# Optimization experiments

Measured on AMD Instinct MI355X. Metric: run time of the kernel, lower is better.

The kernel has to match this reference:

```python
import jax, jax.numpy as jnp
import numpy as np

B, S, HID = 1, 4096, 2304
NH, NKV, HD = 8, 4, 256
SW = 2048                 # sliding window (layer_idx=0 -> active)
SOFTCAP = 50.0
SCALE = 256.0 ** -0.5     # query_pre_attn_scalar ** -0.5
THETA = 10000.0
NEG = -1e30


def rotate_half(x):
    x1, x2 = jnp.split(x, 2, axis=-1)
    return jnp.concatenate([-x2, x1], axis=-1)


def setup_inputs() -> dict:
    key = jax.random.key(0)
    ks = jax.random.split(key, 5)
    hidden_states = jax.random.normal(ks[0], (B, S, HID), jnp.float32)
    position_ids = jnp.tile(jnp.arange(S, dtype=jnp.int32)[None, :], (B, 1))
    Wq = 0.02 * jax.random.normal(ks[1], (NH * HD, HID), jnp.float32)
    Wk = 0.02 * jax.random.normal(ks[2], (NKV * HD, HID), jnp.float32)
    Wv = 0.02 * jax.random.normal(ks[3], (NKV * HD, HID), jnp.float32)
    Wo = 0.02 * jax.random.normal(ks[4], (HID, NH * HD), jnp.float32)
    return {"hidden_states": hidden_states, "position_ids": position_ids,
            "Wq": Wq, "Wk": Wk, "Wv": Wv, "Wo": Wo}


def reference(hidden_states, position_ids, Wq, Wk, Wv, Wo):
    b, s, _ = hidden_states.shape
    # fused QKV projections (torch Linear: y = x @ W.T)
    q = jnp.einsum('bsh,oh->bso', hidden_states, Wq).reshape(b, s, NH, HD).transpose(0, 2, 1, 3)
    k = jnp.einsum('bsh,oh->bso', hidden_states, Wk).reshape(b, s, NKV, HD).transpose(0, 2, 1, 3)
    v = jnp.einsum('bsh,oh->bso', hidden_states, Wv).reshape(b, s, NKV, HD).transpose(0, 2, 1, 3)

    # rotary embedding
    inv_freq = 1.0 / (THETA ** (jnp.arange(0, HD, 2, dtype=jnp.float32) / HD))
    freqs = position_ids.astype(jnp.float32)[:, :, None] * inv_freq[None, None, :]  # [b,s,hd/2]
    emb = jnp.concatenate([freqs, freqs], axis=-1)                                  # [b,s,hd]
    cos = jnp.cos(emb)[:, None, :, :]  # [b,1,s,hd]
    sin = jnp.sin(emb)[:, None, :, :]
    q = q * cos + rotate_half(q) * sin
    k = k * cos + rotate_half(k) * sin

    # GQA: repeat kv heads
    groups = NH // NKV
    k = jnp.repeat(k, groups, axis=1)  # [b,nh,s,hd]
    v = jnp.repeat(v, groups, axis=1)

    scores = jnp.einsum('bhqd,bhkd->bhqk', q, k) * SCALE
    scores = SOFTCAP * jnp.tanh(scores / SOFTCAP)  # logit softcapping

    i = jnp.arange(s)[:, None]
    j = jnp.arange(s)[None, :]
    mask = (j <= i) & ((i - j) < SW)               # causal + sliding window
    scores = jnp.where(mask[None, None], scores, NEG)

    attn = jax.nn.softmax(scores, axis=-1)
    out = jnp.einsum('bhqk,bhkd->bhqd', attn, v)
    out = out.transpose(0, 2, 1, 3).reshape(b, s, NH * HD)
    return jnp.einsum('bso,ho->bsh', out, Wo)
```

## Files before the change

kernel.cpp:

```cpp
#include <hip/hip_runtime.h>
#include <hip/hip_bf16.h>

typedef __attribute__((ext_vector_type(8))) short short8;
typedef __attribute__((ext_vector_type(4))) short short4v;
typedef __attribute__((ext_vector_type(4))) float floatx4;
typedef __attribute__((ext_vector_type(8))) _Float16 half8;

#define S_LEN 4096
#define HIDDEN 2304
#define NHEADS 8
#define NKVH 4
#define HDIM 256
#define SWIN 2048

static __device__ __forceinline__ short bf16bits(float x) {
    __hip_bfloat16 h = __float2bfloat16(x);
    return __builtin_bit_cast(short, h);
}
static __device__ __forceinline__ float bits2f(short b) {
    return __bfloat162float(__builtin_bit_cast(__hip_bfloat16, b));
}

static __device__ __forceinline__ void gload_lds16(const short* g, short* l) {
    __builtin_amdgcn_global_load_lds((const __attribute__((address_space(1))) void*)g,
                                     (__attribute__((address_space(3))) void*)l,
                                     16, 0, 0);
}

__global__ __launch_bounds__(256) void cast_f32_bf16(const float* __restrict__ in,
                                                     short* __restrict__ out, int n4) {
    int i = blockIdx.x * 256 + threadIdx.x;
    if (i >= n4) return;
    float4 v = ((const float4*)in)[i];
    short4v o;
    o.x = bf16bits(v.x); o.y = bf16bits(v.y); o.z = bf16bits(v.z); o.w = bf16bits(v.w);
    ((short4v*)out)[i] = o;
}

__global__ __launch_bounds__(256) void cast_wqkv(const float* __restrict__ Wq,
                                                 const float* __restrict__ Wk,
                                                 const float* __restrict__ Wv,
                                                 short* __restrict__ dst) {
    const int NQ4 = 1179648, NK4 = 589824;
    int i = blockIdx.x * 256 + threadIdx.x;
    const float4* src;
    if (i < NQ4)            src = (const float4*)Wq + i;
    else if (i < NQ4 + NK4) src = (const float4*)Wk + (i - NQ4);
    else                    src = (const float4*)Wv + (i - NQ4 - NK4);
    float4 v = *src;
    short4v o;
    o.x = bf16bits(v.x); o.y = bf16bits(v.y); o.z = bf16bits(v.z); o.w = bf16bits(v.w);
    ((short4v*)dst)[i] = o;
}

template<int MODE>
__global__ __launch_bounds__(256) void gemm_lds(const short* __restrict__ A,
                                                const short* __restrict__ B,
                                                void* __restrict__ Cp,
                                                int M, int N, int K, int ldc)
{
    __shared__ __align__(16) short lA[128 * 32];
    __shared__ __align__(16) short lB[128 * 32];
    int tid  = threadIdx.x;
    int lane = tid & 63;
    int wave = tid >> 6;
    int col  = lane & 15;
    int quad = lane >> 4;
    int m_base = blockIdx.y * 128;
    int n_base = blockIdx.x * 128;
    int wm = (wave >> 1) * 64;
    int wn = (wave & 1) * 64;

    int srow = wave * 32 + (lane >> 2);
    int scol = (lane & 3) * 8;
    const short* gA0 = A + (size_t)(m_base + srow) * K + scol;
    const short* gA1 = gA0 + (size_t)16 * K;
    const short* gB0 = B + (size_t)(n_base + srow) * K + scol;
    const short* gB1 = gB0 + (size_t)16 * K;
    short* lA0 = lA + wave * 1024;
    short* lB0 = lB + wave * 1024;

    floatx4 acc[4][4] = {};

    for (int k0 = 0; k0 < K; k0 += 32) {
        __syncthreads();
        gload_lds16(gA0 + k0, lA0);
        gload_lds16(gA1 + k0, lA0 + 512);
        gload_lds16(gB0 + k0, lB0);
        gload_lds16(gB1 + k0, lB0 + 512);
        __syncthreads();

        short8 af[4], bf[4];
        #pragma unroll
        for (int t = 0; t < 4; ++t) {
            af[t] = *(const short8*)(lA + (wm + t*16 + col) * 32 + quad * 8);
            bf[t] = *(const short8*)(lB + (wn + t*16 + col) * 32 + quad * 8);
        }
        #pragma unroll
        for (int mt = 0; mt < 4; ++mt)
            #pragma unroll
            for (int nt = 0; nt < 4; ++nt)
                acc[mt][nt] = __builtin_amdgcn_mfma_f32_16x16x32_bf16(af[mt], bf[nt], acc[mt][nt], 0, 0, 0);
    }

    #pragma unroll
    for (int mt = 0; mt < 4; ++mt) {
        #pragma unroll
        for (int nt = 0; nt < 4; ++nt) {
            int n  = n_base + wn + nt*16 + col;
            int m0 = m_base + wm + mt*16 + quad*4;
            if (MODE == 0) {
                short* C = (short*)Cp;
                #pragma unroll
                for (int r = 0; r < 4; ++r)
                    C[(size_t)(m0 + r) * ldc + n] = bf16bits(acc[mt][nt][r]);
            } else {
                float* C = (float*)Cp;
                #pragma unroll
                for (int r = 0; r < 4; ++r)
                    C[(size_t)(m0 + r) * ldc + n] = acc[mt][nt][r];
            }
        }
    }
}

__global__ __launch_bounds__(256) void gemm_qkv(const short* __restrict__ A,
                                                const short* __restrict__ B,
                                                short* __restrict__ QKV,
                                                short* __restrict__ Vt)
{
    __shared__ __align__(16) short lA[128 * 32];
    __shared__ __align__(16) short lB[128 * 32];
    const int K = HIDDEN;
    int tid  = threadIdx.x;
    int lane = tid & 63;
    int wave = tid >> 6;
    int col  = lane & 15;
    int quad = lane >> 4;
    int m_base = blockIdx.y * 128;
    int n_base = blockIdx.x * 128;
    int wm = (wave >> 1) * 64;
    int wn = (wave & 1) * 64;

    int srow = wave * 32 + (lane >> 2);
    int scol = (lane & 3) * 8;
    const short* gA0 = A + (size_t)(m_base + srow) * K + scol;
    const short* gA1 = gA0 + (size_t)16 * K;
    const short* gB0 = B + (size_t)(n_base + srow) * K + scol;
    const short* gB1 = gB0 + (size_t)16 * K;
    short* lA0 = lA + wave * 1024;
    short* lB0 = lB + wave * 1024;

    floatx4 acc[4][4] = {};

    for (int k0 = 0; k0 < K; k0 += 32) {
        __syncthreads();
        gload_lds16(gA0 + k0, lA0);
        gload_lds16(gA1 + k0, lA0 + 512);
        gload_lds16(gB0 + k0, lB0);
        gload_lds16(gB1 + k0, lB0 + 512);
        __syncthreads();

        short8 af[4], bf[4];
        #pragma unroll
        for (int t = 0; t < 4; ++t) {
            af[t] = *(const short8*)(lA + (wm + t*16 + col) * 32 + quad * 8);
            bf[t] = *(const short8*)(lB + (wn + t*16 + col) * 32 + quad * 8);
        }
        #pragma unroll
        for (int mt = 0; mt < 4; ++mt)
            #pragma unroll
            for (int nt = 0; nt < 4; ++nt)
                acc[mt][nt] = __builtin_amdgcn_mfma_f32_16x16x32_bf16(af[mt], bf[nt], acc[mt][nt], 0, 0, 0);
    }

    #pragma unroll
    for (int mt = 0; mt < 4; ++mt) {
        #pragma unroll
        for (int nt = 0; nt < 4; ++nt) {
            int n  = n_base + wn + nt*16 + col;
            int m0 = m_base + wm + mt*16 + quad*4;
            if (n_base + wn + nt*16 < 3072) {
                #pragma unroll
                for (int r = 0; r < 4; ++r)
                    QKV[(size_t)(m0 + r) * 4096 + n] = bf16bits(acc[mt][nt][r]);
            } else {
                short4v v;
                v.x = bf16bits(acc[mt][nt][0]);
                v.y = bf16bits(acc[mt][nt][1]);
                v.z = bf16bits(acc[mt][nt][2]);
                v.w = bf16bits(acc[mt][nt][3]);
                *(short4v*)(Vt + (size_t)(n - 3072) * 4096 + m0) = v;
            }
        }
    }
}

__global__ __launch_bounds__(256) void rope_kernel(short* __restrict__ QKV,
                                                   const int* __restrict__ pos)
{
    int t = blockIdx.x * 256 + threadIdx.x;
    int d   = t & 127;
    int rem = t >> 7;
    int hh  = rem % 12;
    int s   = rem / 12;
    float p   = (float)pos[s];
    float inv = __expf(-9.210340371976184f * ((float)d * (1.0f/128.0f)));
    float ang = p * inv;
    float sn, cs;
    sincosf(ang, &sn, &cs);
    short* row = QKV + (size_t)s * 4096 + hh * 256;
    float x1 = bits2f(row[d]);
    float x2 = bits2f(row[d + 128]);
    row[d]       = bf16bits(x1 * cs - x2 * sn);
    row[d + 128] = bf16bits(x2 * cs + x1 * sn);
}

__global__ __launch_bounds__(512) void attn_kernel(const short* __restrict__ QKV,
                                                   const short* __restrict__ Vt,
                                                   _Float16* __restrict__ Opart,
                                                   float* __restrict__ Psp)
{
    __shared__ __align__(16) short lK[2][32 * 256];
    __shared__ __align__(16) short lV[2][256 * 32];
    __shared__ __align__(16) short lP[8][32 * 64];
    int tid  = threadIdx.x;
    int lane = tid & 63;
    int wave = tid >> 6;
    int col  = lane & 15;
    int quad = lane >> 4;
    int bid0 = blockIdx.x;
    int bid  = (bid0 & 7) * 32 + (bid0 >> 3);
    int g     = bid >> 6;
    int chunk = (bid >> 1) & 31;
    int half  = bid & 1;
    int h     = g * 2 + (wave >> 2);
    int qb = chunk * 128;
    int q0 = qb + (wave & 3) * 32;

    short* lPw = lP[wave];

    short8 qf[2][8];
    #pragma unroll
    for (int mt = 0; mt < 2; ++mt) {
        const short* Qrow = QKV + (size_t)(q0 + mt*16 + col) * 4096 + h * 256;
        #pragma unroll
        for (int c = 0; c < 8; ++c)
            qf[mt][c] = *(const short8*)(Qrow + c*32 + quad*8);
    }

    int l5 = lane >> 5;
    int segK = lane & 31;
    const short* pK[2];
    int dKoff[2];
    #pragma unroll
    for (int i = 0; i < 2; ++i) {
        int p = wave * 2 + i;
        int row = 2 * p + l5;
        pK[i] = QKV + (size_t)row * 4096 + 2048 + g * 256 + ((segK ^ (row & 7)) << 3);
        dKoff[i] = p * 512;
    }
    const short* pV[2];
    int dVoff[2];
    #pragma unroll
    for (int i = 0; i < 2; ++i) {
        int row = wave * 32 + i * 16 + (lane >> 2);
        pV[i] = Vt + (size_t)(g * 256 + row) * 4096 + (((lane & 3) ^ ((row >> 1) & 3)) << 3);
        dVoff[i] = wave * 1024 + i * 512;
    }

    floatx4 o[2][16] = {};
    float psum[2][4] = {};

    int kb_lo = qb - (SWIN - 1);
    if (kb_lo < 0) kb_lo = 0;
    kb_lo &= ~31;
    int T  = ((qb + 128) - kb_lo) >> 5;
    int T0 = T >> 1;
    int kb_beg = kb_lo + (half ? T0 * 32 : 0);
    int kb_end = kb_lo + (half ? T * 32 : T0 * 32);

    #pragma unroll
    for (int i = 0; i < 2; ++i)
        gload_lds16(pK[i] + (size_t)kb_beg * 4096, &lK[0][dKoff[i]]);
    #pragma unroll
    for (int i = 0; i < 2; ++i)
        gload_lds16(pV[i] + kb_beg, &lV[0][dVoff[i]]);
    __syncthreads();

    int cur = 0;
    for (int kb = kb_beg; kb < kb_end; kb += 32) {
        int nkb = kb + 32;
        if (nkb < kb_end) {
            #pragma unroll
            for (int i = 0; i < 2; ++i)
                gload_lds16(pK[i] + (size_t)nkb * 4096, &lK[cur ^ 1][dKoff[i]]);
            #pragma unroll
            for (int i = 0; i < 2; ++i)
                gload_lds16(pV[i] + nkb, &lV[cur ^ 1][dVoff[i]]);
        }

        bool deadv = (kb > q0 + 31) || (kb + 2078 < q0);
        if (!deadv) {
            bool full = (kb + 32 <= q0) && (kb >= q0 - 2016);
            const short* Kb = lK[cur];
            const short* Vb = lV[cur];

            floatx4 sc[2][2] = {};
            __builtin_amdgcn_s_setprio(1);
            #pragma unroll
            for (int c = 0; c < 8; ++c) {
                int off = (c*32 + quad*8) ^ ((col & 7) << 3);
                short8 kf0 = *(const short8*)(Kb + col * 256 + off);
                short8 kf1 = *(const short8*)(Kb + (16 + col) * 256 + off);
                #pragma unroll
                for (int mt = 0; mt < 2; ++mt) {
                    sc[mt][0] = __builtin_amdgcn_mfma_f32_16x16x32_bf16(qf[mt][c], kf0, sc[mt][0], 0, 0, 0);
                    sc[mt][1] = __builtin_amdgcn_mfma_f32_16x16x32_bf16(qf[mt][c], kf1, sc[mt][1], 0, 0, 0);
                }
            }
            __builtin_amdgcn_s_setprio(0);

#define CONV_BODY(MASKED)                                                           \
            _Pragma("unroll")                                                       \
            for (int mt = 0; mt < 2; ++mt)                                          \
                _Pragma("unroll")                                                   \
                for (int t = 0; t < 2; ++t)                                         \
                    _Pragma("unroll")                                               \
                    for (int r = 0; r < 4; ++r) {                                   \
                        float y  = sc[mt][t][r] * 0.0625f;                          \
                        float x2 = y * y * 4.0e-4f;                                 \
                        float sv = y * (1.0f + x2 * (-0.33333333f + x2 * 0.13333333f)); \
                        float p  = __expf(sv - 12.0f);                              \
                        int kcol = t*16 + col;                                      \
                        if (MASKED) {                                               \
                            int i = q0 + mt*16 + quad*4 + r;                        \
                            int j = kb + kcol;                                      \
                            bool vv = (j <= i) && ((i - j) < SWIN);                 \
                            p = vv ? p : 0.0f;                                      \
                        }                                                           \
                        psum[mt][r] += p;                                           \
                        int q = mt*16 + quad*4 + r;                                 \
                        lPw[q*64 + (kcol ^ ((q & 7) << 3))] = bf16bits(p);          \
                    }
            if (full) { CONV_BODY(false) } else { CONV_BODY(true) }
#undef CONV_BODY

            __threadfence_block();

            short8 pa[2];
            #pragma unroll
            for (int mt = 0; mt < 2; ++mt)
                pa[mt] = *(const short8*)(&lPw[(mt*16 + col) * 64
                                               + ((quad*8) ^ ((col & 7) << 3))]);

            __builtin_amdgcn_s_setprio(1);
            #pragma unroll
            for (int nt = 0; nt < 16; ++nt) {
                short8 vf = *(const short8*)(Vb + (nt*16 + col) * 32
                                                + ((quad*8) ^ (((col >> 1) & 3) << 3)));
                #pragma unroll
                for (int mt = 0; mt < 2; ++mt)
                    o[mt][nt] = __builtin_amdgcn_mfma_f32_16x16x32_bf16(pa[mt], vf, o[mt][nt], 0, 0, 0);
            }
            __builtin_amdgcn_s_setprio(0);
        }

        __syncthreads();
        cur ^= 1;
    }

    #pragma unroll
    for (int off = 1; off < 16; off <<= 1)
        #pragma unroll
        for (int mt = 0; mt < 2; ++mt)
            #pragma unroll
            for (int r = 0; r < 4; ++r)
                psum[mt][r] += __shfl_xor(psum[mt][r], off, 64);

    _Float16* Op = Opart + (size_t)half * (4096 * 2048);
    #pragma unroll
    for (int mt = 0; mt < 2; ++mt)
        #pragma unroll
        for (int nt = 0; nt < 16; ++nt)
            #pragma unroll
            for (int r = 0; r < 4; ++r) {
                int i = q0 + mt*16 + quad*4 + r;
                Op[(size_t)i * 2048 + h*256 + nt*16 + col] = (_Float16)o[mt][nt][r];
            }
    if (col == 0) {
        #pragma unroll
        for (int mt = 0; mt < 2; ++mt)
            #pragma unroll
            for (int r = 0; r < 4; ++r)
                Psp[half * 32768 + h * 4096 + q0 + mt*16 + quad*4 + r] = psum[mt][r];
    }
}

__global__ __launch_bounds__(256) void combine_kernel(const _Float16* __restrict__ O0,
                                                      const _Float16* __restrict__ O1,
                                                      const float* __restrict__ Ps,
                                                      short* __restrict__ Ob)
{
    int t = blockIdx.x * 256 + threadIdx.x;
    size_t base = (size_t)t * 8;
    int q = (int)(base >> 11);
    int h = (int)((base >> 8) & 7);
    float inv = 1.0f / (Ps[h * 4096 + q] + Ps[32768 + h * 4096 + q]);
    half8 a = *(const half8*)(O0 + base);
    half8 b = *(const half8*)(O1 + base);
    short8 o;
    #pragma unroll
    for (int j = 0; j < 8; ++j)
        o[j] = bf16bits(((float)a[j] + (float)b[j]) * inv);
    *(short8*)(Ob + base) = o;
}

extern "C" void kernel_launch(void* const* d_in, const int* in_sizes, int n_in,
                              void* d_out, int out_size, void* d_ws, size_t ws_size,
                              hipStream_t stream)
{
    const float* X  = (const float*)d_in[0];
    const int*  pos = (const int*)d_in[1];
    const float* Wq = (const float*)d_in[2];
    const float* Wk = (const float*)d_in[3];
    const float* Wv = (const float*)d_in[4];
    const float* Wo = (const float*)d_in[5];
    float* out = (float*)d_out;
    char* ws = (char*)d_ws;

    short* Xb    = (short*)(ws + 0);
    short* Wqkvb = (short*)(ws + 18874368);
    short* Wob   = (short*)(ws + 37748736);
    short* QKVb  = (short*)(ws + 47185920);
    short* Vt    = (short*)(ws + 80740352);
    _Float16* Opart = (_Float16*)(ws + 0);
    float*    Psp   = (float*)(ws + 33554432);
    short*    Ob    = (short*)(ws + 0);

    cast_f32_bf16<<<9216, 256, 0, stream>>>(X,  Xb,  2359296);
    cast_wqkv<<<9216, 256, 0, stream>>>(Wq, Wk, Wv, Wqkvb);
    cast_f32_bf16<<<4608, 256, 0, stream>>>(Wo, Wob, 1179648);

    gemm_qkv<<<dim3(32,32), 256, 0, stream>>>(Xb, Wqkvb, QKVb, Vt);

    rope_kernel<<<24576, 256, 0, stream>>>(QKVb, pos);

    attn_kernel<<<256, 512, 0, stream>>>(QKVb, Vt, Opart, Psp);

    combine_kernel<<<4096, 256, 0, stream>>>(Opart, Opart + (size_t)4096*2048, Psp, Ob);

    gemm_lds<2><<<dim3(18,32), 256, 0, stream>>>(Ob, Wob, out, 4096, 2304, 2048, 2304);
}
```

Measured before the change: 483.2 us.

## Shrink attention blocks to 64 queries and drop LDS double buffering for occupancy

The attention kernel moves from 512-thread blocks covering 128 queries to 256-thread blocks covering 64 queries, with twice as many blocks and launch bounds requesting two blocks per CU. The K/V LDS double buffer becomes a single buffer loaded synchronously inside each iteration with barriers on both sides. This halves LDS use per block and aims for better CU fill and latency hiding across resident blocks. The cost is that K/V tiles are reloaded from global by twice as many blocks and each block loses intra-block prefetch overlap.

```diff
diff --git a/kernel.cpp b/kernel.cpp
--- a/kernel.cpp
+++ b/kernel.cpp
@@ -216,27 +216,28 @@
     row[d + 128] = bf16bits(x2 * cs + x1 * sn);
 }
 
-__global__ __launch_bounds__(512) void attn_kernel(const short* __restrict__ QKV,
-                                                   const short* __restrict__ Vt,
-                                                   _Float16* __restrict__ Opart,
-                                                   float* __restrict__ Psp)
-{
-    __shared__ __align__(16) short lK[2][32 * 256];
-    __shared__ __align__(16) short lV[2][256 * 32];
-    __shared__ __align__(16) short lP[8][32 * 64];
+__global__ __launch_bounds__(256, 2) void attn_kernel(const short* __restrict__ QKV,
+                                                      const short* __restrict__ Vt,
+                                                      _Float16* __restrict__ Opart,
+                                                      float* __restrict__ Psp)
+{
+    __shared__ __align__(16) short lK[32 * 256];
+    __shared__ __align__(16) short lV[256 * 32];
+    __shared__ __align__(16) short lP[4][32 * 64];
     int tid  = threadIdx.x;
     int lane = tid & 63;
     int wave = tid >> 6;
     int col  = lane & 15;
     int quad = lane >> 4;
     int bid0 = blockIdx.x;
-    int bid  = (bid0 & 7) * 32 + (bid0 >> 3);
-    int g     = bid >> 6;
-    int chunk = (bid >> 1) & 31;
-    int half  = bid & 1;
-    int h     = g * 2 + (wave >> 2);
-    int qb = chunk * 128;
-    int q0 = qb + (wave & 3) * 32;
+    int x = bid0 & 7;
+    int s = bid0 >> 3;
+    int g     = x >> 1;
+    int chunk = ((s >> 1) << 1) | (x & 1);
+    int half  = s & 1;
+    int h     = g * 2 + (wave >> 1);
+    int qb = chunk * 64;
+    int q0 = qb + (wave & 1) * 32;
 
     short* lPw = lP[wave];
 
@@ -251,23 +252,18 @@
 
     int l5 = lane >> 5;
     int segK = lane & 31;
-    const short* pK[2];
-    int dKoff[2];
-    #pragma unroll
-    for (int i = 0; i < 2; ++i) {
-        int p = wave * 2 + i;
-        int row = 2 * p + l5;
-        pK[i] = QKV + (size_t)row * 4096 + 2048 + g * 256 + ((segK ^ (row & 7)) << 3);
-        dKoff[i] = p * 512;
-    }
-    const short* pV[2];
-    int dVoff[2];
-    #pragma unroll
-    for (int i = 0; i < 2; ++i) {
-        int row = wave * 32 + i * 16 + (lane >> 2);
-        pV[i] = Vt + (size_t)(g * 256 + row) * 4096 + (((lane & 3) ^ ((row >> 1) & 3)) << 3);
-        dVoff[i] = wave * 1024 + i * 512;
-    }
+    const short* pK[4];
+    int dKoff[4];
+    #pragma unroll
+    for (int j = 0; j < 4; ++j) {
+        int row = wave * 8 + 2 * j + l5;
+        pK[j] = QKV + (size_t)row * 4096 + 2048 + g * 256 + ((segK ^ (row & 7)) << 3);
+        dKoff[j] = (wave * 8 + 2 * j) * 256;
+    }
+    int rowV = wave * 64 + (lane >> 2);
+    const short* pV = Vt + (size_t)(g * 256 + rowV) * 4096
+                        + (((lane & 3) ^ ((rowV >> 1) & 3)) << 3);
+    int dVbase = wave * 64 * 32;
 
     floatx4 o[2][16] = {};
     float psum[2][4] = {};
@@ -275,44 +271,32 @@
     int kb_lo = qb - (SWIN - 1);
     if (kb_lo < 0) kb_lo = 0;
     kb_lo &= ~31;
-    int T  = ((qb + 128) - kb_lo) >> 5;
+    int T  = ((qb + 64) - kb_lo) >> 5;
     int T0 = T >> 1;
     int kb_beg = kb_lo + (half ? T0 * 32 : 0);
     int kb_end = kb_lo + (half ? T * 32 : T0 * 32);
 
-    #pragma unroll
-    for (int i = 0; i < 2; ++i)
-        gload_lds16(pK[i] + (size_t)kb_beg * 4096, &lK[0][dKoff[i]]);
-    #pragma unroll
-    for (int i = 0; i < 2; ++i)
-        gload_lds16(pV[i] + kb_beg, &lV[0][dVoff[i]]);
-    __syncthreads();
-
-    int cur = 0;
     for (int kb = kb_beg; kb < kb_end; kb += 32) {
-        int nkb = kb + 32;
-        if (nkb < kb_end) {
-            #pragma unroll
-            for (int i = 0; i < 2; ++i)
-                gload_lds16(pK[i] + (size_t)nkb * 4096, &lK[cur ^ 1][dKoff[i]]);
-            #pragma unroll
-            for (int i = 0; i < 2; ++i)
-                gload_lds16(pV[i] + nkb, &lV[cur ^ 1][dVoff[i]]);
-        }
+        __syncthreads();
+        #pragma unroll
+        for (int j = 0; j < 4; ++j)
+            gload_lds16(pK[j] + (size_t)kb * 4096, lK + dKoff[j]);
+        #pragma unroll
+        for (int i = 0; i < 4; ++i)
+            gload_lds16(pV + (size_t)(16 * i) * 4096 + kb, lV + dVbase + i * 512);
+        __syncthreads();
 
         bool deadv = (kb > q0 + 31) || (kb + 2078 < q0);
         if (!deadv) {
             bool full = (kb + 32 <= q0) && (kb >= q0 - 2016);
-            const short* Kb = lK[cur];
-            const short* Vb = lV[cur];
 
             floatx4 sc[2][2] = {};
             __builtin_amdgcn_s_setprio(1);
             #pragma unroll
             for (int c = 0; c < 8; ++c) {
                 int off = (c*32 + quad*8) ^ ((col & 7) << 3);
-                short8 kf0 = *(const short8*)(Kb + col * 256 + off);
-                short8 kf1 = *(const short8*)(Kb + (16 + col) * 256 + off);
+                short8 kf0 = *(const short8*)(lK + col * 256 + off);
+                short8 kf1 = *(const short8*)(lK + (16 + col) * 256 + off);
                 #pragma unroll
                 for (int mt = 0; mt < 2; ++mt) {
                     sc[mt][0] = __builtin_amdgcn_mfma_f32_16x16x32_bf16(qf[mt][c], kf0, sc[mt][0], 0, 0, 0);
@@ -357,7 +341,7 @@
             __builtin_amdgcn_s_setprio(1);
             #pragma unroll
             for (int nt = 0; nt < 16; ++nt) {
-                short8 vf = *(const short8*)(Vb + (nt*16 + col) * 32
+                short8 vf = *(const short8*)(lV + (nt*16 + col) * 32
                                                 + ((quad*8) ^ (((col >> 1) & 3) << 3)));
                 #pragma unroll
                 for (int mt = 0; mt < 2; ++mt)
@@ -365,9 +349,6 @@
             }
             __builtin_amdgcn_s_setprio(0);
         }
-
-        __syncthreads();
-        cur ^= 1;
     }
 
     #pragma unroll
@@ -446,7 +427,7 @@
 
     rope_kernel<<<24576, 256, 0, stream>>>(QKVb, pos);
 
-    attn_kernel<<<256, 512, 0, stream>>>(QKVb, Vt, Opart, Psp);
+    attn_kernel<<<512, 256, 0, stream>>>(QKVb, Vt, Opart, Psp);
 
     combine_kernel<<<4096, 256, 0, stream>>>(Opart, Opart + (size_t)4096*2048, Psp, Ob);
 
```

New measurement: 486.5 us. No clear change (+0.7%).
